# Kernel optimization log

Hardware: AMD Instinct MI355X
Metric: run time of the kernel (lower is better)

## Reference

```python
import jax, jax.numpy as jnp
import numpy as np

B_, D_, L_, N_ = 2, 1536, 2048, 16


def setup_inputs() -> dict:
    key = jax.random.key(0)
    ks = jax.random.split(key, 8)
    x = jax.random.normal(ks[0], (B_, D_, L_), dtype=jnp.float32)
    delta = jax.random.normal(ks[1], (B_, D_, L_), dtype=jnp.float32)
    # A negative (as in Mamba, A = -exp(A_log)) so the recurrence is stable
    A = -(jax.random.uniform(ks[2], (D_, N_), dtype=jnp.float32) + 0.5)
    B = jax.random.normal(ks[3], (B_, N_, L_), dtype=jnp.float32)
    C = jax.random.normal(ks[4], (B_, N_, L_), dtype=jnp.float32)
    D = jax.random.normal(ks[5], (D_,), dtype=jnp.float32)
    z = jax.random.normal(ks[6], (B_, D_, L_), dtype=jnp.float32)
    delta_bias = jax.random.normal(ks[7], (D_,), dtype=jnp.float32)
    return {"x": x, "delta": delta, "A": A, "B": B, "C": C,
            "D": D, "z": z, "delta_bias": delta_bias}


def reference(x, delta, A, B, C, D, z, delta_bias):
    # delta_softplus=True path with delta_bias, variable B (bnl) and C (bnl)
    delta = jax.nn.softplus(delta + delta_bias[None, :, None])      # (b,d,l)
    deltaA = jnp.exp(jnp.einsum('bdl,dn->bdln', delta, A))          # (b,d,l,n)
    deltaB_x = jnp.einsum('bdl,bnl,bdl->bdln', delta, B, x)         # (b,d,l,n)

    # scan over the sequence axis: h = deltaA_t * h + deltaB_x_t; y = h @ C_t
    dA_t = jnp.transpose(deltaA, (2, 0, 1, 3))     # (l,b,d,n)
    dBx_t = jnp.transpose(deltaB_x, (2, 0, 1, 3))  # (l,b,d,n)
    C_t = jnp.transpose(C, (2, 0, 1))              # (l,b,n)

    def step(h, inp):
        dA_i, dBx_i, C_i = inp
        h = dA_i * h + dBx_i                       # (b,d,n)
        y = jnp.einsum('bdn,bn->bd', h, C_i)       # (b,d)
        return h, y

    h0 = jnp.zeros((x.shape[0], A.shape[0], A.shape[1]), dtype=jnp.float32)
    _, ys = jax.lax.scan(step, h0, (dA_t, dBx_t, C_t))  # ys: (l,b,d)
    y = jnp.transpose(ys, (1, 2, 0))                    # (b,d,l)

    out = y + x * D[None, :, None]                      # D skip connection
    out = out * (z * jax.nn.sigmoid(z))                 # SiLU gate
    return out
```

## Files before the change

kernel.cpp:

```cpp
#include <hip/hip_runtime.h>
#include <math.h>

#define B_  2
#define D_  1536
#define L_  2048
#define N_  16
#define NH  8
#define LC  128
#define NCHUNK (L_ / LC)
#define NCH (B_ * D_)
#define LOG2E 1.4426950408889634f
#define LN2   0.6931471805599453f

typedef float f4 __attribute__((ext_vector_type(4)));
typedef float f8 __attribute__((ext_vector_type(8)));

__device__ __forceinline__ float exp2f_(float v) { return __builtin_amdgcn_exp2f(v); }
__device__ __forceinline__ float log2f_(float v) { return __builtin_amdgcn_logf(v); }
__device__ __forceinline__ float rcpf_(float v)  { return __builtin_amdgcn_rcpf(v); }

__device__ __forceinline__ float softplus_f(float v) {
    float t = exp2f_(v * LOG2E);
    float r = LN2 * log2f_(1.0f + t);
    return (v > 20.0f) ? v : r;
}
__device__ __forceinline__ f8 splat8(float v) { f8 r = {v,v,v,v,v,v,v,v}; return r; }
__device__ __forceinline__ f8 exp2v8(f8 a) {
    f8 r;
    r[0]=exp2f_(a[0]); r[1]=exp2f_(a[1]); r[2]=exp2f_(a[2]); r[3]=exp2f_(a[3]);
    r[4]=exp2f_(a[4]); r[5]=exp2f_(a[5]); r[6]=exp2f_(a[6]); r[7]=exp2f_(a[7]);
    return r;
}
__device__ __forceinline__ float dot8(f8 a, f8 b) {
    float p0 = fmaf(a[0], b[0], a[1]*b[1]);
    float p1 = fmaf(a[2], b[2], a[3]*b[3]);
    float p2 = fmaf(a[4], b[4], a[5]*b[5]);
    float p3 = fmaf(a[6], b[6], a[7]*b[7]);
    return (p0 + p1) + (p2 + p3);
}

#define DPP_ROW_SHR(N) (0x110 + (N))
#define DPP_ROW_BCAST15 0x142
#define DPP_WAVE_SHR1   0x138
template<int CTRL, int RMASK>
__device__ __forceinline__ float updpp(float old, float v) {
    return __int_as_float(__builtin_amdgcn_update_dpp(
        __float_as_int(old), __float_as_int(v), CTRL, RMASK, 0xF, false));
}

__global__ __launch_bounds__(64, 3)
void ssm_scan_kernel(const float* __restrict__ x,
                     const float* __restrict__ delta,
                     const float* __restrict__ A,
                     const float* __restrict__ Bm,
                     const float* __restrict__ Cm,
                     const float* __restrict__ Dv,
                     const float* __restrict__ z,
                     const float* __restrict__ dbias,
                     float* __restrict__ out)
{
    const int lane = threadIdx.x;
    const int s    = lane & 31;
    const int g    = lane >> 5;
    const int ch   = blockIdx.x;
    const int b    = ch / D_;
    const int d    = ch - b * D_;

    const float bias = dbias[d];
    const float Dd   = Dv[d];

    const float* Ab = A + d * N_ + NH * g;
    f8 A2v;
    A2v[0]=Ab[0]*LOG2E; A2v[1]=Ab[1]*LOG2E; A2v[2]=Ab[2]*LOG2E; A2v[3]=Ab[3]*LOG2E;
    A2v[4]=Ab[4]*LOG2E; A2v[5]=Ab[5]*LOG2E; A2v[6]=Ab[6]*LOG2E; A2v[7]=Ab[7]*LOG2E;

    const float* Bp = Bm + (size_t)b * (N_ * L_) + (size_t)(NH * g) * L_;
    const float* Cp = Cm + (size_t)b * (N_ * L_) + (size_t)(NH * g) * L_;
    const size_t chbase = (size_t)ch * L_;

    f8 carry = splat8(0.0f);

    for (int c = 0; c < NCHUNK; ++c) {
        const int off = c * LC + s * 4;

        f4 dv = *(const f4*)(delta + chbase + off);
        f4 xv = *(const f4*)(x     + chbase + off);
        f4 zv = *(const f4*)(z     + chbase + off);
#define LD_BC(i) f4 Bv##i = *(const f4*)(Bp + i * L_ + off); \
                 f4 Cv##i = *(const f4*)(Cp + i * L_ + off);
        LD_BC(0) LD_BC(1) LD_BC(2) LD_BC(3) LD_BC(4) LD_BC(5) LD_BC(6) LD_BC(7)

        float dt0 = softplus_f(dv.x + bias);
        float dt1 = softplus_f(dv.y + bias);
        float dt2 = softplus_f(dv.z + bias);
        float dt3 = softplus_f(dv.w + bias);
        float u0 = dt0 * xv.x, u1 = dt1 * xv.y, u2 = dt2 * xv.z, u3 = dt3 * xv.w;
        float dtsum = (dt0 + dt1) + (dt2 + dt3);

        f8 e0 = exp2v8(splat8(dt0) * A2v);
        f8 e1 = exp2v8(splat8(dt1) * A2v);
        f8 e2 = exp2v8(splat8(dt2) * A2v);
        f8 e3 = exp2v8(splat8(dt3) * A2v);
        f8 P  = exp2v8(splat8(dtsum) * A2v);

        f8 tB0 = {Bv0.x,Bv1.x,Bv2.x,Bv3.x,Bv4.x,Bv5.x,Bv6.x,Bv7.x};
        f8 tB1 = {Bv0.y,Bv1.y,Bv2.y,Bv3.y,Bv4.y,Bv5.y,Bv6.y,Bv7.y};
        f8 tB2 = {Bv0.z,Bv1.z,Bv2.z,Bv3.z,Bv4.z,Bv5.z,Bv6.z,Bv7.z};
        f8 tB3 = {Bv0.w,Bv1.w,Bv2.w,Bv3.w,Bv4.w,Bv5.w,Bv6.w,Bv7.w};
        f8 uB0 = splat8(u0) * tB0;
        f8 uB1 = splat8(u1) * tB1;
        f8 uB2 = splat8(u2) * tB2;
        f8 uB3 = splat8(u3) * tB3;
        f8 SC0 = {Cv0.x,Cv1.x,Cv2.x,Cv3.x,Cv4.x,Cv5.x,Cv6.x,Cv7.x};
        f8 SC1 = {Cv0.y,Cv1.y,Cv2.y,Cv3.y,Cv4.y,Cv5.y,Cv6.y,Cv7.y};
        f8 SC2 = {Cv0.z,Cv1.z,Cv2.z,Cv3.z,Cv4.z,Cv5.z,Cv6.z,Cv7.z};
        f8 SC3 = {Cv0.w,Cv1.w,Cv2.w,Cv3.w,Cv4.w,Cv5.w,Cv6.w,Cv7.w};

        f8 S = uB0;
        S = e1 * S + uB1;
        S = e2 * S + uB2;
        S = e3 * S + uB3;

#define SCAN_STEP(CTRL, RMASK) \
        { \
            _Pragma("unroll") \
            for (int i = 0; i < NH; ++i) { \
                float Pp = updpp<CTRL, RMASK>(1.0f, P[i]); \
                float Sp = updpp<CTRL, RMASK>(0.0f, S[i]); \
                S[i] = fmaf(Sp, P[i], S[i]);    \
                P[i] = P[i] * Pp; \
            } \
        }
        SCAN_STEP(DPP_ROW_SHR(1), 0xF)
        SCAN_STEP(DPP_ROW_SHR(2), 0xF)
        SCAN_STEP(DPP_ROW_SHR(4), 0xF)
        SCAN_STEP(DPP_ROW_SHR(8), 0xF)
        SCAN_STEP(DPP_ROW_BCAST15, 0xA)

        f8 h;
#pragma unroll
        for (int i = 0; i < NH; ++i) {
            float hinc = fmaf(carry[i], P[i], S[i]);
            float hup  = updpp<DPP_WAVE_SHR1, 0xF>(0.0f, hinc);
            h[i] = (s == 0) ? carry[i] : hup;
            carry[i] = __shfl(hinc, 31, 32);
        }

        h = e0 * h + uB0;  float y0 = dot8(h, SC0);
        h = e1 * h + uB1;  float y1 = dot8(h, SC1);
        h = e2 * h + uB2;  float y2 = dot8(h, SC2);
        h = e3 * h + uB3;  float y3 = dot8(h, SC3);

        y0 += __shfl_xor(y0, 32, 64);
        y1 += __shfl_xor(y1, 32, 64);
        y2 += __shfl_xor(y2, 32, 64);
        y3 += __shfl_xor(y3, 32, 64);
        if (g == 0) {
            float s0 = rcpf_(1.0f + exp2f_(-zv.x * LOG2E));
            float s1 = rcpf_(1.0f + exp2f_(-zv.y * LOG2E));
            float s2 = rcpf_(1.0f + exp2f_(-zv.z * LOG2E));
            float s3 = rcpf_(1.0f + exp2f_(-zv.w * LOG2E));
            f4 ov = { (y0 + xv.x * Dd) * (zv.x * s0),
                      (y1 + xv.y * Dd) * (zv.y * s1),
                      (y2 + xv.z * Dd) * (zv.z * s2),
                      (y3 + xv.w * Dd) * (zv.w * s3) };
            *(f4*)(out + chbase + off) = ov;
        }
    }
}

extern "C" void kernel_launch(void* const* d_in, const int* in_sizes, int n_in,
                              void* d_out, int out_size, void* d_ws, size_t ws_size,
                              hipStream_t stream) {
    const float* x     = (const float*)d_in[0];
    const float* delta = (const float*)d_in[1];
    const float* A     = (const float*)d_in[2];
    const float* Bm    = (const float*)d_in[3];
    const float* Cm    = (const float*)d_in[4];
    const float* Dv    = (const float*)d_in[5];
    const float* z     = (const float*)d_in[6];
    const float* dbias = (const float*)d_in[7];
    float* out = (float*)d_out;

    dim3 grid(NCH);
    dim3 block(64);
    ssm_scan_kernel<<<grid, block, 0, stream>>>(x, delta, A, Bm, Cm, Dv, z, dbias, out);
}
```

Measured before the change: 173.4 us.

## Split state dims across two waves and double chunk length per iteration

Each block now uses two 64-lane wavefronts, one per half of the 16 state dimensions, and each wave covers a 256-element chunk with a full 64-lane DPP scan (an extra row_bcast31 step). The two partial y values are combined through a double-buffered shared-memory array and a block barrier, replacing the cross-half shuffle. Delta and x for the next chunk are prefetched one iteration ahead, and only the first wave loads z. The aim is more work per scan step and more latency hiding, at the cost of a __syncthreads per chunk and a deeper scan.

```diff
diff --git a/kernel.cpp b/kernel.cpp
--- a/kernel.cpp
+++ b/kernel.cpp
@@ -6,7 +6,7 @@
 #define L_  2048
 #define N_  16
 #define NH  8
-#define LC  128
+#define LC  256
 #define NCHUNK (L_ / LC)
 #define NCH (B_ * D_)
 #define LOG2E 1.4426950408889634f
@@ -41,6 +41,7 @@
 
 #define DPP_ROW_SHR(N) (0x110 + (N))
 #define DPP_ROW_BCAST15 0x142
+#define DPP_ROW_BCAST31 0x143
 #define DPP_WAVE_SHR1   0x138
 template<int CTRL, int RMASK>
 __device__ __forceinline__ float updpp(float old, float v) {
@@ -48,7 +49,7 @@
         __float_as_int(old), __float_as_int(v), CTRL, RMASK, 0xF, false));
 }
 
-__global__ __launch_bounds__(64, 3)
+__global__ __launch_bounds__(128, 6)
 void ssm_scan_kernel(const float* __restrict__ x,
                      const float* __restrict__ delta,
                      const float* __restrict__ A,
@@ -59,36 +60,44 @@
                      const float* __restrict__ dbias,
                      float* __restrict__ out)
 {
-    const int lane = threadIdx.x;
-    const int s    = lane & 31;
-    const int g    = lane >> 5;
+    const int tid  = threadIdx.x;
+    const int lane = tid & 63;
+    const int w    = tid >> 6;
     const int ch   = blockIdx.x;
     const int b    = ch / D_;
     const int d    = ch - b * D_;
 
+    __shared__ f4 ybuf[2][64];
+
     const float bias = dbias[d];
     const float Dd   = Dv[d];
 
-    const float* Ab = A + d * N_ + NH * g;
+    const float* Ab = A + d * N_ + NH * w;
     f8 A2v;
     A2v[0]=Ab[0]*LOG2E; A2v[1]=Ab[1]*LOG2E; A2v[2]=Ab[2]*LOG2E; A2v[3]=Ab[3]*LOG2E;
     A2v[4]=Ab[4]*LOG2E; A2v[5]=Ab[5]*LOG2E; A2v[6]=Ab[6]*LOG2E; A2v[7]=Ab[7]*LOG2E;
 
-    const float* Bp = Bm + (size_t)b * (N_ * L_) + (size_t)(NH * g) * L_;
-    const float* Cp = Cm + (size_t)b * (N_ * L_) + (size_t)(NH * g) * L_;
+    const float* Bp = Bm + (size_t)b * (N_ * L_) + (size_t)(NH * w) * L_;
+    const float* Cp = Cm + (size_t)b * (N_ * L_) + (size_t)(NH * w) * L_;
     const size_t chbase = (size_t)ch * L_;
 
     f8 carry = splat8(0.0f);
 
+    f4 dv = *(const f4*)(delta + chbase + lane * 4);
+    f4 xv = *(const f4*)(x     + chbase + lane * 4);
+
     for (int c = 0; c < NCHUNK; ++c) {
-        const int off = c * LC + s * 4;
-
-        f4 dv = *(const f4*)(delta + chbase + off);
-        f4 xv = *(const f4*)(x     + chbase + off);
-        f4 zv = *(const f4*)(z     + chbase + off);
+        const int off  = c * LC + lane * 4;
+        const int offn = ((c + 1) & (NCHUNK - 1)) * LC + lane * 4;
+
+        f4 zv = {0.0f, 0.0f, 0.0f, 0.0f};
+        if (w == 0) zv = *(const f4*)(z + chbase + off);
 #define LD_BC(i) f4 Bv##i = *(const f4*)(Bp + i * L_ + off); \
                  f4 Cv##i = *(const f4*)(Cp + i * L_ + off);
         LD_BC(0) LD_BC(1) LD_BC(2) LD_BC(3) LD_BC(4) LD_BC(5) LD_BC(6) LD_BC(7)
+
+        f4 dvn = *(const f4*)(delta + chbase + offn);
+        f4 xvn = *(const f4*)(x     + chbase + offn);
 
         float dt0 = softplus_f(dv.x + bias);
         float dt1 = softplus_f(dv.y + bias);
@@ -136,14 +145,15 @@
         SCAN_STEP(DPP_ROW_SHR(4), 0xF)
         SCAN_STEP(DPP_ROW_SHR(8), 0xF)
         SCAN_STEP(DPP_ROW_BCAST15, 0xA)
+        SCAN_STEP(DPP_ROW_BCAST31, 0xC)
 
         f8 h;
 #pragma unroll
         for (int i = 0; i < NH; ++i) {
             float hinc = fmaf(carry[i], P[i], S[i]);
             float hup  = updpp<DPP_WAVE_SHR1, 0xF>(0.0f, hinc);
-            h[i] = (s == 0) ? carry[i] : hup;
-            carry[i] = __shfl(hinc, 31, 32);
+            h[i] = (lane == 0) ? carry[i] : hup;
+            carry[i] = __shfl(hinc, 63, 64);
         }
 
         h = e0 * h + uB0;  float y0 = dot8(h, SC0);
@@ -151,21 +161,24 @@
         h = e2 * h + uB2;  float y2 = dot8(h, SC2);
         h = e3 * h + uB3;  float y3 = dot8(h, SC3);
 
-        y0 += __shfl_xor(y0, 32, 64);
-        y1 += __shfl_xor(y1, 32, 64);
-        y2 += __shfl_xor(y2, 32, 64);
-        y3 += __shfl_xor(y3, 32, 64);
-        if (g == 0) {
+        if (w == 1) {
+            f4 yv = { y0, y1, y2, y3 };
+            ybuf[c & 1][lane] = yv;
+        }
+        __syncthreads();
+        if (w == 0) {
+            f4 yo = ybuf[c & 1][lane];
             float s0 = rcpf_(1.0f + exp2f_(-zv.x * LOG2E));
             float s1 = rcpf_(1.0f + exp2f_(-zv.y * LOG2E));
             float s2 = rcpf_(1.0f + exp2f_(-zv.z * LOG2E));
             float s3 = rcpf_(1.0f + exp2f_(-zv.w * LOG2E));
-            f4 ov = { (y0 + xv.x * Dd) * (zv.x * s0),
-                      (y1 + xv.y * Dd) * (zv.y * s1),
-                      (y2 + xv.z * Dd) * (zv.z * s2),
-                      (y3 + xv.w * Dd) * (zv.w * s3) };
+            f4 ov = { (y0 + yo.x + xv.x * Dd) * (zv.x * s0),
+                      (y1 + yo.y + xv.y * Dd) * (zv.y * s1),
+                      (y2 + yo.z + xv.z * Dd) * (zv.z * s2),
+                      (y3 + yo.w + xv.w * Dd) * (zv.w * s3) };
             *(f4*)(out + chbase + off) = ov;
         }
+        dv = dvn; xv = xvn;
     }
 }
 
@@ -183,6 +196,6 @@
     float* out = (float*)d_out;
 
     dim3 grid(NCH);
-    dim3 block(64);
+    dim3 block(128);
     ssm_scan_kernel<<<grid, block, 0, stream>>>(x, delta, A, Bm, Cm, Dv, z, dbias, out);
 }
```

Measured after the change: 187.2 us. 1.08x slower.

## Split each channel's chunks across two waves with an LDS carry handoff

Applied to the files above, without the earlier changes.

Each block now runs two wavefronts that process alternating 128-step chunks of the same channel. The sequential carry is passed between them through shared memory, guarded by two barriers per chunk pair. The per-lane local scan is reorganised to track cumulative decay products (F) and partial outputs, so output y needs only dot products with the incoming state instead of re-running the recurrence. The intent is more parallelism per channel and fewer exp evaluations (the separate dtsum exp is removed), at the cost of barrier serialization and extra register pressure.

```diff
diff --git a/kernel.cpp b/kernel.cpp
--- a/kernel.cpp
+++ b/kernel.cpp
@@ -47,8 +47,13 @@
     return __int_as_float(__builtin_amdgcn_update_dpp(
         __float_as_int(old), __float_as_int(v), CTRL, RMASK, 0xF, false));
 }
-
-__global__ __launch_bounds__(64, 3)
+template<int CTRL, int RMASK>
+__device__ __forceinline__ float dpp0(float v) {
+    return __int_as_float(__builtin_amdgcn_update_dpp(
+        0, __float_as_int(v), CTRL, RMASK, 0xF, true));
+}
+
+__global__ __launch_bounds__(128, 5)
 void ssm_scan_kernel(const float* __restrict__ x,
                      const float* __restrict__ delta,
                      const float* __restrict__ A,
@@ -59,12 +64,17 @@
                      const float* __restrict__ dbias,
                      float* __restrict__ out)
 {
-    const int lane = threadIdx.x;
+    const int tid  = threadIdx.x;
+    const int lane = tid & 63;
     const int s    = lane & 31;
-    const int g    = lane >> 5;
+    const int g    = (lane >> 5) & 1;
+    const int w    = tid >> 6;
     const int ch   = blockIdx.x;
     const int b    = ch / D_;
     const int d    = ch - b * D_;
+
+    __shared__ alignas(16) float carrybuf[2][N_];
+    if (tid < 2 * N_) ((float*)carrybuf)[tid] = 0.0f;
 
     const float bias = dbias[d];
     const float Dd   = Dv[d];
@@ -78,79 +88,127 @@
     const float* Cp = Cm + (size_t)b * (N_ * L_) + (size_t)(NH * g) * L_;
     const size_t chbase = (size_t)ch * L_;
 
-    f8 carry = splat8(0.0f);
-
-    for (int c = 0; c < NCHUNK; ++c) {
+    __syncthreads();
+
+#define SCAN_STEP_F(CTRL) \
+    { \
+        _Pragma("unroll") \
+        for (int i = 0; i < NH; ++i) { \
+            float Pp = updpp<CTRL, 0xF>(1.0f, F3v[i]); \
+            float Sp = dpp0<CTRL, 0xF>(S3v[i]); \
+            S3v[i] = fmaf(Sp, F3v[i], S3v[i]);    \
+            F3v[i] = F3v[i] * Pp; \
+        } \
+    }
+#define SCAN_STEP_M(CTRL, RMASK) \
+    { \
+        _Pragma("unroll") \
+        for (int i = 0; i < NH; ++i) { \
+            float Pp = updpp<CTRL, RMASK>(1.0f, F3v[i]); \
+            float Sp = updpp<CTRL, RMASK>(0.0f, S3v[i]); \
+            S3v[i] = fmaf(Sp, F3v[i], S3v[i]); \
+            F3v[i] = F3v[i] * Pp; \
+        } \
+    }
+#define FOLDCORE \
+    { \
+        _Pragma("unroll") \
+        for (int i = 0; i < NH; ++i) { \
+            hincv[i] = fmaf(cin[i], F3v[i], S3v[i]); \
+            float hup = dpp0<DPP_WAVE_SHR1, 0xF>(hincv[i]);  \
+            h[i] = (s == 0) ? cin[i] : hup;                  \
+        } \
+        if (s == 31) { \
+            f4 lo = { hincv[0], hincv[1], hincv[2], hincv[3] }; \
+            f4 hi = { hincv[4], hincv[5], hincv[6], hincv[7] }; \
+            *(f4*)&carrybuf[w][g * NH]     = lo; \
+            *(f4*)&carrybuf[w][g * NH + 4] = hi; \
+        } \
+    }
+#define LDS_CIN(SLOT) \
+    { \
+        f4 lo = *(const f4*)&carrybuf[SLOT][g * NH]; \
+        f4 hi = *(const f4*)&carrybuf[SLOT][g * NH + 4]; \
+        cin[0]=lo.x; cin[1]=lo.y; cin[2]=lo.z; cin[3]=lo.w; \
+        cin[4]=hi.x; cin[5]=hi.y; cin[6]=hi.z; cin[7]=hi.w; \
+    }
+
+    for (int k = 0; k < NCHUNK / 2; ++k) {
+        const int c   = 2 * k + w;
         const int off = c * LC + s * 4;
 
-        f4 dv = *(const f4*)(delta + chbase + off);
-        f4 xv = *(const f4*)(x     + chbase + off);
-        f4 zv = *(const f4*)(z     + chbase + off);
-#define LD_BC(i) f4 Bv##i = *(const f4*)(Bp + i * L_ + off); \
-                 f4 Cv##i = *(const f4*)(Cp + i * L_ + off);
-        LD_BC(0) LD_BC(1) LD_BC(2) LD_BC(3) LD_BC(4) LD_BC(5) LD_BC(6) LD_BC(7)
+        f4 dv  = *(const f4*)(delta + chbase + off);
+        f4 xv  = *(const f4*)(x     + chbase + off);
+        f4 Bv0 = *(const f4*)(Bp + 0 * L_ + off);
+        f4 Bv1 = *(const f4*)(Bp + 1 * L_ + off);
+        f4 Bv2 = *(const f4*)(Bp + 2 * L_ + off);
+        f4 Bv3 = *(const f4*)(Bp + 3 * L_ + off);
+        f4 Bv4 = *(const f4*)(Bp + 4 * L_ + off);
+        f4 Bv5 = *(const f4*)(Bp + 5 * L_ + off);
+        f4 Bv6 = *(const f4*)(Bp + 6 * L_ + off);
+        f4 Bv7 = *(const f4*)(Bp + 7 * L_ + off);
+        f4 Cv0 = *(const f4*)(Cp + 0 * L_ + off);
+        f4 Cv1 = *(const f4*)(Cp + 1 * L_ + off);
+        f4 Cv2 = *(const f4*)(Cp + 2 * L_ + off);
+        f4 Cv3 = *(const f4*)(Cp + 3 * L_ + off);
+        f4 Cv4 = *(const f4*)(Cp + 4 * L_ + off);
+        f4 Cv5 = *(const f4*)(Cp + 5 * L_ + off);
+        f4 Cv6 = *(const f4*)(Cp + 6 * L_ + off);
+        f4 Cv7 = *(const f4*)(Cp + 7 * L_ + off);
 
         float dt0 = softplus_f(dv.x + bias);
         float dt1 = softplus_f(dv.y + bias);
         float dt2 = softplus_f(dv.z + bias);
         float dt3 = softplus_f(dv.w + bias);
-        float u0 = dt0 * xv.x, u1 = dt1 * xv.y, u2 = dt2 * xv.z, u3 = dt3 * xv.w;
-        float dtsum = (dt0 + dt1) + (dt2 + dt3);
+        float u0 = dt0 * xv.x, u1 = dt1 * xv.y;
+        float u2 = dt2 * xv.z, u3 = dt3 * xv.w;
 
         f8 e0 = exp2v8(splat8(dt0) * A2v);
         f8 e1 = exp2v8(splat8(dt1) * A2v);
         f8 e2 = exp2v8(splat8(dt2) * A2v);
         f8 e3 = exp2v8(splat8(dt3) * A2v);
-        f8 P  = exp2v8(splat8(dtsum) * A2v);
 
         f8 tB0 = {Bv0.x,Bv1.x,Bv2.x,Bv3.x,Bv4.x,Bv5.x,Bv6.x,Bv7.x};
         f8 tB1 = {Bv0.y,Bv1.y,Bv2.y,Bv3.y,Bv4.y,Bv5.y,Bv6.y,Bv7.y};
         f8 tB2 = {Bv0.z,Bv1.z,Bv2.z,Bv3.z,Bv4.z,Bv5.z,Bv6.z,Bv7.z};
         f8 tB3 = {Bv0.w,Bv1.w,Bv2.w,Bv3.w,Bv4.w,Bv5.w,Bv6.w,Bv7.w};
-        f8 uB0 = splat8(u0) * tB0;
-        f8 uB1 = splat8(u1) * tB1;
-        f8 uB2 = splat8(u2) * tB2;
-        f8 uB3 = splat8(u3) * tB3;
+
+        f8 S0v = splat8(u0) * tB0;             f8 F0v = e0;
+        f8 S1v = e1 * S0v + splat8(u1) * tB1;  f8 F1v = e1 * F0v;
+        f8 S2v = e2 * S1v + splat8(u2) * tB2;  f8 F2v = e2 * F1v;
+        f8 S3v = e3 * S2v + splat8(u3) * tB3;  f8 F3v = e3 * F2v;
+
         f8 SC0 = {Cv0.x,Cv1.x,Cv2.x,Cv3.x,Cv4.x,Cv5.x,Cv6.x,Cv7.x};
         f8 SC1 = {Cv0.y,Cv1.y,Cv2.y,Cv3.y,Cv4.y,Cv5.y,Cv6.y,Cv7.y};
         f8 SC2 = {Cv0.z,Cv1.z,Cv2.z,Cv3.z,Cv4.z,Cv5.z,Cv6.z,Cv7.z};
         f8 SC3 = {Cv0.w,Cv1.w,Cv2.w,Cv3.w,Cv4.w,Cv5.w,Cv6.w,Cv7.w};
-
-        f8 S = uB0;
-        S = e1 * S + uB1;
-        S = e2 * S + uB2;
-        S = e3 * S + uB3;
-
-#define SCAN_STEP(CTRL, RMASK) \
-        { \
-            _Pragma("unroll") \
-            for (int i = 0; i < NH; ++i) { \
-                float Pp = updpp<CTRL, RMASK>(1.0f, P[i]); \
-                float Sp = updpp<CTRL, RMASK>(0.0f, S[i]); \
-                S[i] = fmaf(Sp, P[i], S[i]);    \
-                P[i] = P[i] * Pp; \
-            } \
+        float y00 = dot8(SC0, S0v);  f8 G0 = SC0 * F0v;
+        float y10 = dot8(SC1, S1v);  f8 G1 = SC1 * F1v;
+        float y20 = dot8(SC2, S2v);  f8 G2 = SC2 * F2v;
+
+        SCAN_STEP_F(DPP_ROW_SHR(1))
+        SCAN_STEP_F(DPP_ROW_SHR(2))
+        SCAN_STEP_F(DPP_ROW_SHR(4))
+        SCAN_STEP_F(DPP_ROW_SHR(8))
+        SCAN_STEP_M(DPP_ROW_BCAST15, 0xA)
+
+        f8 cin, h, hincv;
+        __syncthreads();
+        if (w == 0) {
+            LDS_CIN(1)
+            FOLDCORE
         }
-        SCAN_STEP(DPP_ROW_SHR(1), 0xF)
-        SCAN_STEP(DPP_ROW_SHR(2), 0xF)
-        SCAN_STEP(DPP_ROW_SHR(4), 0xF)
-        SCAN_STEP(DPP_ROW_SHR(8), 0xF)
-        SCAN_STEP(DPP_ROW_BCAST15, 0xA)
-
-        f8 h;
-#pragma unroll
-        for (int i = 0; i < NH; ++i) {
-            float hinc = fmaf(carry[i], P[i], S[i]);
-            float hup  = updpp<DPP_WAVE_SHR1, 0xF>(0.0f, hinc);
-            h[i] = (s == 0) ? carry[i] : hup;
-            carry[i] = __shfl(hinc, 31, 32);
+        __syncthreads();
+        if (w == 1) {
+            LDS_CIN(0)
+            FOLDCORE
         }
 
-        h = e0 * h + uB0;  float y0 = dot8(h, SC0);
-        h = e1 * h + uB1;  float y1 = dot8(h, SC1);
-        h = e2 * h + uB2;  float y2 = dot8(h, SC2);
-        h = e3 * h + uB3;  float y3 = dot8(h, SC3);
-
+        f4 zv = *(const f4*)(z + chbase + off);
+        float y0 = y00 + dot8(G0, h);
+        float y1 = y10 + dot8(G1, h);
+        float y2 = y20 + dot8(G2, h);
+        float y3 = dot8(SC3, hincv);
         y0 += __shfl_xor(y0, 32, 64);
         y1 += __shfl_xor(y1, 32, 64);
         y2 += __shfl_xor(y2, 32, 64);
@@ -183,6 +241,6 @@
     float* out = (float*)d_out;
 
     dim3 grid(NCH);
-    dim3 block(64);
+    dim3 block(128);
     ssm_scan_kernel<<<grid, block, 0, stream>>>(x, delta, A, Bm, Cm, Dv, z, dbias, out);
 }
```

After: 364.4 us. +110.2%, slower.
